# Performance work log

Hardware: AMD Instinct MI355X
Metric: run time of the kernel (lower is better)

## Reference

```python
import jax, jax.numpy as jnp
import numpy as np

B, L, H, N, VOCAB, OUT, NL = 16, 2048, 512, 64, 256, 256, 4
N2 = N // 2  # conjugate-symmetric half of the state


def setup_inputs() -> dict:
    key = jax.random.key(0)
    ks = jax.random.split(key, 8)
    x = jax.random.randint(ks[0], (B, L), 0, VOCAB)
    emb = jax.random.normal(ks[1], (VOCAB, H), jnp.float32)
    Ws = jax.random.normal(ks[2], (NL, H, H), jnp.float32) / np.float32(np.sqrt(H))
    bs = jnp.zeros((NL, H), jnp.float32)
    dt_min, dt_max = 1e-3, 1e-1
    log_dt = (jax.random.uniform(ks[3], (NL, H), jnp.float32)
              * np.float32(np.log(dt_max) - np.log(dt_min)) + np.float32(np.log(dt_min)))
    log_A_real = jnp.full((NL, H, N2), np.float32(np.log(0.5)), jnp.float32)
    A_imag = jnp.broadcast_to(np.float32(np.pi) * jnp.arange(N2, dtype=jnp.float32), (NL, H, N2))
    C_re = jax.random.normal(ks[4], (NL, H, N2), jnp.float32)
    C_im = jax.random.normal(ks[5], (NL, H, N2), jnp.float32)
    Ds = jax.random.normal(ks[6], (NL, H), jnp.float32)
    Wo = jax.random.normal(ks[7], (H, OUT), jnp.float32) / np.float32(np.sqrt(H))
    bo = jnp.zeros((OUT,), jnp.float32)
    return dict(x=x, emb=emb, Ws=Ws, bs=bs, log_dt=log_dt, log_A_real=log_A_real,
                A_imag=A_imag, C_re=C_re, C_im=C_im, Ds=Ds, Wo=Wo, bo=bo)


def _s4d(u, log_dt, log_A_real, A_imag, C_re, C_im, D):
    # u: (B, Lseq, H). Standard minimal S4D (diagonal SSM, ZOH-style kernel, FFT causal conv).
    Lseq = u.shape[1]
    dt = jnp.exp(log_dt)                      # (H,)
    A = -jnp.exp(log_A_real) + 1j * A_imag    # (H, N2) complex
    C = C_re + 1j * C_im                      # (H, N2)
    dtA = A * dt[:, None]                     # (H, N2)
    coef = C * (jnp.exp(dtA) - 1.0) / A       # (H, N2)
    # Vandermonde over time: exp(dtA * l), l = 0..L-1
    vand = jnp.exp(dtA[:, :, None] * jnp.arange(Lseq, dtype=jnp.float32))  # (H, N2, L)
    K = 2.0 * jnp.einsum('hn,hnl->hl', coef, vand).real                    # (H, L)
    ud = jnp.transpose(u, (0, 2, 1))          # (B, H, L)
    kf = jnp.fft.rfft(K, n=2 * Lseq)
    uf = jnp.fft.rfft(ud, n=2 * Lseq)
    y = jnp.fft.irfft(uf * kf, n=2 * Lseq)[..., :Lseq]  # causal conv
    y = y + D[:, None] * ud                   # skip connection
    return jnp.transpose(y, (0, 2, 1))        # (B, L, H)


def reference(x, emb, Ws, bs, log_dt, log_A_real, A_imag, C_re, C_im, Ds, Wo, bo):
    h = emb[x]  # (B, L, H)
    for i in range(NL):
        # every sub-layer gets the outer residual: x = layer(x) + x
        h = (h @ Ws[i] + bs[i]) + h           # Linear + residual
        h = jax.nn.relu(h) + h                # ReLU + residual
        h = h + h                             # Dropout (eval: identity) + residual
        h = _s4d(h, log_dt[i], log_A_real[i], A_imag[i], C_re[i], C_im[i], Ds[i]) + h
        h = jax.nn.relu(h) + h
        h = h + h
    return h @ Wo + bo
```

## Files before the change

### kernel.cpp

```cpp
#include <hip/hip_runtime.h>

#define BB 16
#define LL 2048
#define HH 512
#define NN2 32
#define NLAY 4
#define OUTD 256
#define BLM (BB*LL)
#define NELEM ((size_t)BLM*HH)
#define NC 16
#define LC (LL/NC)
#define LGLC 7

typedef __attribute__((ext_vector_type(8))) short s8v;
typedef __attribute__((ext_vector_type(4))) float f4v;

__device__ __forceinline__ unsigned short f2bf(float f) {
  unsigned u = __float_as_uint(f);
  return (unsigned short)((u + 0x7fffu + ((u >> 16) & 1u)) >> 16);
}
__device__ __forceinline__ float bf2f(unsigned short h) {
  return __uint_as_float((unsigned)h << 16);
}
__device__ __forceinline__ void gload16(const void* g, void* l) {
  __builtin_amdgcn_global_load_lds(
      (const __attribute__((address_space(1))) unsigned int*)g,
      (__attribute__((address_space(3))) unsigned int*)l, 16, 0, 0);
}

__global__ __launch_bounds__(256) void k_embed(const int* __restrict__ x,
    const float* __restrict__ emb, unsigned short* __restrict__ Ahi,
    unsigned short* __restrict__ Alo) {
  int idx = blockIdx.x * 256 + threadIdx.x;
  int j4 = idx & 127;
  int bl = idx >> 7;
  int tok = x[bl];
  float4 v = reinterpret_cast<const float4*>(emb)[tok * 128 + j4];
  unsigned short h0 = f2bf(v.x), h1 = f2bf(v.y), h2 = f2bf(v.z), h3 = f2bf(v.w);
  unsigned short l0 = f2bf(v.x - bf2f(h0)), l1 = f2bf(v.y - bf2f(h1));
  unsigned short l2 = f2bf(v.z - bf2f(h2)), l3 = f2bf(v.w - bf2f(h3));
  uint2 hp = make_uint2((unsigned)h0 | ((unsigned)h1 << 16),
                        (unsigned)h2 | ((unsigned)h3 << 16));
  uint2 lp = make_uint2((unsigned)l0 | ((unsigned)l1 << 16),
                        (unsigned)l2 | ((unsigned)l3 << 16));
  *reinterpret_cast<uint2*>(&Ahi[(size_t)idx * 4]) = hp;
  *reinterpret_cast<uint2*>(&Alo[(size_t)idx * 4]) = lp;
}

__global__ __launch_bounds__(256) void k_trans(const float* __restrict__ W, int N,
    unsigned short* __restrict__ th, unsigned short* __restrict__ tl) {
  int t = blockIdx.x * 256 + threadIdx.x;
  int k = t & 511, n = t >> 9;
  float v = W[(size_t)k * N + n];
  unsigned short hi = f2bf(v);
  th[(size_t)n * 512 + k] = hi;
  tl[(size_t)n * 512 + k] = f2bf(v - bf2f(hi));
}

__global__ __launch_bounds__(256) void k_params(const float* __restrict__ log_dt,
    const float* __restrict__ log_A_real, const float* __restrict__ A_imag,
    const float* __restrict__ C_re, const float* __restrict__ C_im,
    int layer, float4* __restrict__ par) {
  int idx = blockIdx.x * 256 + threadIdx.x;
  int h = idx >> 5;
  int o = layer * HH * NN2 + idx;
  float dt  = expf(log_dt[layer * HH + h]);
  float Are = -expf(log_A_real[o]);
  float Aim = A_imag[o];
  float er = expf(Are * dt);
  float lr = er * cosf(Aim * dt), li = er * sinf(Aim * dt);
  float inv  = 1.0f / (Are * Are + Aim * Aim);
  float numr = lr - 1.0f, numi = li;
  float qr = (numr * Are + numi * Aim) * inv;
  float qi = (numi * Are - numr * Aim) * inv;
  float cr = C_re[o], ci = C_im[o];
  par[idx] = make_float4(lr, li, 2.0f * (cr * qr - ci * qi),
                                 2.0f * (cr * qi + ci * qr));
}

template<int EPI>
__global__ __launch_bounds__(256) void k_gemm(
    const unsigned short* __restrict__ Ahi, const unsigned short* __restrict__ Alo,
    const unsigned short* __restrict__ Bhi, const unsigned short* __restrict__ Blo,
    const float* __restrict__ bias, float* __restrict__ Out, int N) {
  __shared__ short lds[32768];
  const int tid = threadIdx.x;
  const int lane = tid & 63, w = tid >> 6;
  const int wr = w >> 1, wc = w & 1;
  const int m0 = blockIdx.y * 128, n0 = blockIdx.x * 128;
  const int lm = lane & 15, lk = lane >> 4;

  const unsigned short* ga[2][2]; const unsigned short* gb[2][2];
  short *da[2][2], *db[2][2];
#pragma unroll
  for (int f2 = 0; f2 < 2; ++f2) {
    int f = w * 2 + f2;
    size_t ra = (size_t)(m0 + f * 16 + lm) * 512 + lk * 8;
    size_t rb = (size_t)(n0 + f * 16 + lm) * 512 + lk * 8;
    ga[0][f2] = Ahi + ra; ga[1][f2] = Alo + ra;
    gb[0][f2] = Bhi + rb; gb[1][f2] = Blo + rb;
    da[0][f2] = &lds[f * 512 + lane * 8];
    da[1][f2] = &lds[4096 + f * 512 + lane * 8];
    db[0][f2] = &lds[8192 + f * 512 + lane * 8];
    db[1][f2] = &lds[12288 + f * 512 + lane * 8];
  }
  f4v acc[4][4];
#pragma unroll
  for (int i = 0; i < 4; ++i)
#pragma unroll
    for (int j = 0; j < 4; ++j) acc[i][j] = (f4v){0.f, 0.f, 0.f, 0.f};

  auto stage = [&](int kt, int bofs) {
#pragma unroll
    for (int f2 = 0; f2 < 2; ++f2) {
      gload16(ga[0][f2] + kt * 32, da[0][f2] + bofs);
      gload16(ga[1][f2] + kt * 32, da[1][f2] + bofs);
      gload16(gb[0][f2] + kt * 32, db[0][f2] + bofs);
      gload16(gb[1][f2] + kt * 32, db[1][f2] + bofs);
    }
  };
  auto compute = [&](int bofs) {
    s8v ah[4], al[4], bh[4], bl[4];
#pragma unroll
    for (int i = 0; i < 4; ++i) {
      ah[i] = *(const s8v*)&lds[bofs + (wr * 4 + i) * 512 + lane * 8];
      al[i] = *(const s8v*)&lds[bofs + 4096 + (wr * 4 + i) * 512 + lane * 8];
      bh[i] = *(const s8v*)&lds[bofs + 8192 + (wc * 4 + i) * 512 + lane * 8];
      bl[i] = *(const s8v*)&lds[bofs + 12288 + (wc * 4 + i) * 512 + lane * 8];
    }
#pragma unroll
    for (int mi = 0; mi < 4; ++mi)
#pragma unroll
      for (int ni = 0; ni < 4; ++ni) {
        acc[mi][ni] = __builtin_amdgcn_mfma_f32_16x16x32_bf16(ah[mi], bh[ni], acc[mi][ni], 0, 0, 0);
        acc[mi][ni] = __builtin_amdgcn_mfma_f32_16x16x32_bf16(al[mi], bh[ni], acc[mi][ni], 0, 0, 0);
        acc[mi][ni] = __builtin_amdgcn_mfma_f32_16x16x32_bf16(ah[mi], bl[ni], acc[mi][ni], 0, 0, 0);
      }
  };

  stage(0, 0);
  __syncthreads();
#pragma unroll 1
  for (int t = 0; t < 8; ++t) {
    stage(2 * t + 1, 16384);
    compute(0);
    __syncthreads();
    if (t < 7) stage(2 * t + 2, 0);
    compute(16384);
    __syncthreads();
  }
  float bb[4];
#pragma unroll
  for (int ni = 0; ni < 4; ++ni) bb[ni] = bias[n0 + wc * 64 + ni * 16 + lm];
#pragma unroll
  for (int mi = 0; mi < 4; ++mi) {
#pragma unroll
    for (int r = 0; r < 4; ++r) {
      int row = m0 + wr * 64 + mi * 16 + lk * 4 + r;
      float* po = Out + (size_t)row * N;
      const unsigned short* ph = Ahi + (size_t)row * 512;
      const unsigned short* pl = Alo + (size_t)row * 512;
#pragma unroll
      for (int ni = 0; ni < 4; ++ni) {
        int col = n0 + wc * 64 + ni * 16 + lm;
        float t = acc[mi][ni][r] + bb[ni];
        if (EPI) {
          t += bf2f(ph[col]) + bf2f(pl[col]);
          t = t < 0.f ? 2.f * t : 4.f * t;
        }
        po[col] = t;
      }
    }
  }
}

__global__ __launch_bounds__(256) void k_sa(const float* __restrict__ U,
    const float4* __restrict__ par, float2* __restrict__ st) {
  int tid = threadIdx.x;
  int n = tid & 31, hs = tid >> 5;
  int hb = blockIdx.x, c = blockIdx.y, b = blockIdx.z;
  int h = (hb << 3) + hs;
  float4 p = par[(h << 5) + n];
  float lr = p.x, li = p.y;
  const float* Up = U + ((size_t)b * LL + (size_t)c * LC) * HH + h;
  float sr = 0.f, si = 0.f;
  auto step = [&](float uv) {
    float nsr = fmaf(lr, sr, fmaf(-li, si, uv));
    si = fmaf(lr, si, li * sr);
    sr = nsr;
  };
  float u0 = Up[0], u1 = Up[HH], u2 = Up[2 * HH], u3 = Up[3 * HH];
  for (int lg = 0; lg < LC / 4; ++lg) {
    const float* nx = Up + (size_t)(lg * 4 + 4) * HH;
    float v0 = nx[0], v1 = nx[HH], v2 = nx[2 * HH], v3 = nx[3 * HH];
    step(u0); step(u1); step(u2); step(u3);
    u0 = v0; u1 = v1; u2 = v2; u3 = v3;
  }
  st[(((size_t)b * (NC - 1) + c) * HH + h) * NN2 + n] = make_float2(sr, si);
}

__global__ __launch_bounds__(256) void k_fold(const float4* __restrict__ par,
    float2* __restrict__ st) {
  int t = blockIdx.x * 256 + threadIdx.x;
  int hn = t & 16383;
  int b = t >> 14;
  float4 p = par[hn];
  float ar = p.x, ai = p.y;
#pragma unroll
  for (int s = 0; s < LGLC; ++s) { float nr = ar * ar - ai * ai; ai = 2.f * ar * ai; ar = nr; }
  float gr = 0.f, gi = 0.f;
  size_t idx = (size_t)b * (NC - 1) * 16384 + hn;
  for (int c = 0; c < NC - 1; ++c) {
    float2 s = st[idx + (size_t)c * 16384];
    float ngr = fmaf(ar, gr, fmaf(-ai, gi, s.x));
    gi = fmaf(ar, gi, fmaf(ai, gr, s.y));
    gr = ngr;
    st[idx + (size_t)c * 16384] = make_float2(gr, gi);
  }
}

__global__ __launch_bounds__(256) void k_sb(const float* __restrict__ U,
    const float4* __restrict__ par, const float2* __restrict__ st,
    const float* __restrict__ D, unsigned short* __restrict__ Hhi,
    unsigned short* __restrict__ Hlo) {
  int tid = threadIdx.x;
  int q = tid & 3, hs = tid >> 2;
  int hb = blockIdx.x, c = blockIdx.y, b = blockIdx.z;
  int h = (hb << 6) + hs;
  float lr[8], li[8], cr[8], ci[8], tr[8], ti[8];
#pragma unroll
  for (int j = 0; j < 8; ++j) {
    float4 p = par[(h << 5) + (q << 3) + j];
    lr[j] = p.x; li[j] = p.y; cr[j] = p.z; ci[j] = p.w;
    tr[j] = 0.f; ti[j] = 0.f;
  }
  if (c > 0) {
#pragma unroll
    for (int j = 0; j < 8; ++j) {
      float2 s = st[(((size_t)b * (NC - 1) + (c - 1)) * HH + h) * NN2 + (q << 3) + j];
      tr[j] = cr[j] * s.x - ci[j] * s.y;
      ti[j] = cr[j] * s.y + ci[j] * s.x;
    }
  }
  float dp1 = D[h] + 1.0f;
  size_t base = ((size_t)b * LL + (size_t)c * LC) * HH + h;
  const float* Up = U + base;
  auto step = [&](float uv) -> float {
    float ys = 0.f;
#pragma unroll
    for (int j = 0; j < 8; ++j) {
      float ntr = fmaf(lr[j], tr[j], fmaf(-li[j], ti[j], cr[j] * uv));
      ti[j] = fmaf(lr[j], ti[j], fmaf(li[j], tr[j], ci[j] * uv));
      tr[j] = ntr;
      ys += ntr;
    }
    ys += __shfl_xor(ys, 1);
    ys += __shfl_xor(ys, 2);
    float t4 = fmaf(dp1, uv, ys);
    return t4 < 0.f ? 2.f * t4 : 4.f * t4;
  };
  float u0 = Up[0], u1 = Up[HH], u2 = Up[2 * HH], u3 = Up[3 * HH];
  for (int lg = 0; lg < LC / 4; ++lg) {
    const float* nx = Up + (size_t)(lg * 4 + 4) * HH;
    float v0 = nx[0], v1 = nx[HH], v2 = nx[2 * HH], v3 = nx[3 * HH];
    float r0 = step(u0), r1 = step(u1), r2 = step(u2), r3 = step(u3);
    float rq = q == 0 ? r0 : q == 1 ? r1 : q == 2 ? r2 : r3;
    size_t o = base + (size_t)(lg * 4 + q) * HH;
    unsigned short hi = f2bf(rq);
    Hhi[o] = hi;
    Hlo[o] = f2bf(rq - bf2f(hi));
    u0 = v0; u1 = v1; u2 = v2; u3 = v3;
  }
}

extern "C" void kernel_launch(void* const* d_in, const int* in_sizes, int n_in,
                              void* d_out, int out_size, void* d_ws, size_t ws_size,
                              hipStream_t stream) {
  const int*   x      = (const int*)d_in[0];
  const float* emb    = (const float*)d_in[1];
  const float* Ws     = (const float*)d_in[2];
  const float* bs     = (const float*)d_in[3];
  const float* log_dt = (const float*)d_in[4];
  const float* lAr    = (const float*)d_in[5];
  const float* Aim    = (const float*)d_in[6];
  const float* Cre    = (const float*)d_in[7];
  const float* Cim    = (const float*)d_in[8];
  const float* Ds     = (const float*)d_in[9];
  const float* Wo     = (const float*)d_in[10];
  const float* bo     = (const float*)d_in[11];

  float*          bufU   = (float*)d_ws;
  unsigned short* bufAhi = (unsigned short*)(bufU + NELEM);
  unsigned short* bufAlo = bufAhi + NELEM;
  float4*         par    = (float4*)(bufAlo + NELEM);
  float2*         st     = (float2*)(par + HH * NN2);
  unsigned short* wth    = (unsigned short*)(st + (size_t)BB * (NC - 1) * HH * NN2);
  unsigned short* wtl    = wth + 512 * 512;

  k_embed<<<(int)(NELEM / 4 / 256), 256, 0, stream>>>(x, emb, bufAhi, bufAlo);
  for (int i = 0; i < NLAY; ++i) {
    k_params<<<HH * NN2 / 256, 256, 0, stream>>>(log_dt, lAr, Aim, Cre, Cim, i, par);
    k_trans<<<HH * 512 / 256, 256, 0, stream>>>(Ws + (size_t)i * HH * HH, HH, wth, wtl);
    k_gemm<1><<<dim3(HH / 128, BLM / 128), 256, 0, stream>>>(
        bufAhi, bufAlo, wth, wtl, bs + i * HH, bufU, HH);
    k_sa<<<dim3(64, NC - 1, BB), 256, 0, stream>>>(bufU, par, st);
    k_fold<<<BB * HH * NN2 / 256, 256, 0, stream>>>(par, st);
    k_sb<<<dim3(8, NC, BB), 256, 0, stream>>>(bufU, par, st, Ds + i * HH, bufAhi, bufAlo);
  }
  k_trans<<<OUTD * 512 / 256, 256, 0, stream>>>(Wo, OUTD, wth, wtl);
  k_gemm<0><<<dim3(OUTD / 128, BLM / 128), 256, 0, stream>>>(
      bufAhi, bufAlo, wth, wtl, bo, (float*)d_out, OUTD);
}
```

Measured before the change: 1.189 ms.

## Assign all SSM modes of a channel to one thread in scan kernels

The chunked diagonal-SSM scan kernels now give each thread one channel and all 32 complex modes, instead of spreading modes across lanes. The parameter and state layouts become mode-major so per-channel accesses coalesce across threads. This removes redundant input loads and the cross-lane shuffle reduction, and lets each thread write four outputs. The cost is heavy register pressure and far fewer blocks and waves, which reduces latency hiding.

```diff
diff --git a/kernel.cpp b/kernel.cpp
--- a/kernel.cpp
+++ b/kernel.cpp
@@ -62,7 +62,7 @@
     const float* __restrict__ C_re, const float* __restrict__ C_im,
     int layer, float4* __restrict__ par) {
   int idx = blockIdx.x * 256 + threadIdx.x;
-  int h = idx >> 5;
+  int h = idx >> 5, n = idx & 31;
   int o = layer * HH * NN2 + idx;
   float dt  = expf(log_dt[layer * HH + h]);
   float Are = -expf(log_A_real[o]);
@@ -74,8 +74,8 @@
   float qr = (numr * Are + numi * Aim) * inv;
   float qi = (numi * Are - numr * Aim) * inv;
   float cr = C_re[o], ci = C_im[o];
-  par[idx] = make_float4(lr, li, 2.0f * (cr * qr - ci * qi),
-                                 2.0f * (cr * qi + ci * qr));
+  par[n * HH + h] = make_float4(lr, li, 2.0f * (cr * qr - ci * qi),
+                                        2.0f * (cr * qi + ci * qr));
 }
 
 template<int EPI>
@@ -174,20 +174,24 @@
   }
 }
 
-__global__ __launch_bounds__(256) void k_sa(const float* __restrict__ U,
+__global__ __launch_bounds__(256, 2) void k_sa(const float* __restrict__ U,
     const float4* __restrict__ par, float2* __restrict__ st) {
-  int tid = threadIdx.x;
-  int n = tid & 31, hs = tid >> 5;
-  int hb = blockIdx.x, c = blockIdx.y, b = blockIdx.z;
-  int h = (hb << 3) + hs;
-  float4 p = par[(h << 5) + n];
-  float lr = p.x, li = p.y;
+  int h = (blockIdx.x << 8) + threadIdx.x;
+  int c = blockIdx.y, b = blockIdx.z;
+  float lr[32], li[32], gr[32], gi[32];
+#pragma unroll
+  for (int n = 0; n < 32; ++n) {
+    float4 p = par[n * HH + h];
+    lr[n] = p.x; li[n] = p.y; gr[n] = 0.f; gi[n] = 0.f;
+  }
   const float* Up = U + ((size_t)b * LL + (size_t)c * LC) * HH + h;
-  float sr = 0.f, si = 0.f;
   auto step = [&](float uv) {
-    float nsr = fmaf(lr, sr, fmaf(-li, si, uv));
-    si = fmaf(lr, si, li * sr);
-    sr = nsr;
+#pragma unroll
+    for (int n = 0; n < 32; ++n) {
+      float ngr = fmaf(lr[n], gr[n], fmaf(-li[n], gi[n], uv));
+      gi[n] = fmaf(lr[n], gi[n], li[n] * gr[n]);
+      gr[n] = ngr;
+    }
   };
   float u0 = Up[0], u1 = Up[HH], u2 = Up[2 * HH], u3 = Up[3 * HH];
   for (int lg = 0; lg < LC / 4; ++lg) {
@@ -196,20 +200,23 @@
     step(u0); step(u1); step(u2); step(u3);
     u0 = v0; u1 = v1; u2 = v2; u3 = v3;
   }
-  st[(((size_t)b * (NC - 1) + c) * HH + h) * NN2 + n] = make_float2(sr, si);
+  size_t so = ((size_t)b * (NC - 1) + c) * (NN2 * HH) + h;
+#pragma unroll
+  for (int n = 0; n < 32; ++n)
+    st[so + (size_t)n * HH] = make_float2(gr[n], gi[n]);
 }
 
 __global__ __launch_bounds__(256) void k_fold(const float4* __restrict__ par,
     float2* __restrict__ st) {
   int t = blockIdx.x * 256 + threadIdx.x;
-  int hn = t & 16383;
+  int r = t & 16383;
   int b = t >> 14;
-  float4 p = par[hn];
+  float4 p = par[r];
   float ar = p.x, ai = p.y;
 #pragma unroll
   for (int s = 0; s < LGLC; ++s) { float nr = ar * ar - ai * ai; ai = 2.f * ar * ai; ar = nr; }
   float gr = 0.f, gi = 0.f;
-  size_t idx = (size_t)b * (NC - 1) * 16384 + hn;
+  size_t idx = (size_t)b * (NC - 1) * 16384 + r;
   for (int c = 0; c < NC - 1; ++c) {
     float2 s = st[idx + (size_t)c * 16384];
     float ngr = fmaf(ar, gr, fmaf(-ai, gi, s.x));
@@ -219,56 +226,58 @@
   }
 }
 
-__global__ __launch_bounds__(256) void k_sb(const float* __restrict__ U,
+__global__ __launch_bounds__(256, 2) void k_sb(const float* __restrict__ U,
     const float4* __restrict__ par, const float2* __restrict__ st,
     const float* __restrict__ D, unsigned short* __restrict__ Hhi,
     unsigned short* __restrict__ Hlo) {
-  int tid = threadIdx.x;
-  int q = tid & 3, hs = tid >> 2;
-  int hb = blockIdx.x, c = blockIdx.y, b = blockIdx.z;
-  int h = (hb << 6) + hs;
-  float lr[8], li[8], cr[8], ci[8], tr[8], ti[8];
-#pragma unroll
-  for (int j = 0; j < 8; ++j) {
-    float4 p = par[(h << 5) + (q << 3) + j];
-    lr[j] = p.x; li[j] = p.y; cr[j] = p.z; ci[j] = p.w;
-    tr[j] = 0.f; ti[j] = 0.f;
+  int h = (blockIdx.x << 8) + threadIdx.x;
+  int c = blockIdx.y, b = blockIdx.z;
+  float lr[32], li[32], cr[32], ci[32], tr[32], ti[32];
+#pragma unroll
+  for (int n = 0; n < 32; ++n) {
+    float4 p = par[n * HH + h];
+    lr[n] = p.x; li[n] = p.y; cr[n] = p.z; ci[n] = p.w;
+    tr[n] = 0.f; ti[n] = 0.f;
   }
   if (c > 0) {
-#pragma unroll
-    for (int j = 0; j < 8; ++j) {
-      float2 s = st[(((size_t)b * (NC - 1) + (c - 1)) * HH + h) * NN2 + (q << 3) + j];
-      tr[j] = cr[j] * s.x - ci[j] * s.y;
-      ti[j] = cr[j] * s.y + ci[j] * s.x;
+    size_t so = ((size_t)b * (NC - 1) + (c - 1)) * (NN2 * HH) + h;
+#pragma unroll
+    for (int n = 0; n < 32; ++n) {
+      float2 s = st[so + (size_t)n * HH];
+      tr[n] = cr[n] * s.x - ci[n] * s.y;
+      ti[n] = cr[n] * s.y + ci[n] * s.x;
     }
   }
   float dp1 = D[h] + 1.0f;
   size_t base = ((size_t)b * LL + (size_t)c * LC) * HH + h;
   const float* Up = U + base;
+  unsigned short* Hh = Hhi + base;
+  unsigned short* Hl = Hlo + base;
   auto step = [&](float uv) -> float {
-    float ys = 0.f;
-#pragma unroll
-    for (int j = 0; j < 8; ++j) {
-      float ntr = fmaf(lr[j], tr[j], fmaf(-li[j], ti[j], cr[j] * uv));
-      ti[j] = fmaf(lr[j], ti[j], fmaf(li[j], tr[j], ci[j] * uv));
-      tr[j] = ntr;
-      ys += ntr;
-    }
-    ys += __shfl_xor(ys, 1);
-    ys += __shfl_xor(ys, 2);
-    float t4 = fmaf(dp1, uv, ys);
+    float y0 = 0.f, y1 = 0.f, y2 = 0.f, y3 = 0.f;
+#pragma unroll
+    for (int n = 0; n < 32; ++n) {
+      float ntr = fmaf(lr[n], tr[n], fmaf(-li[n], ti[n], cr[n] * uv));
+      ti[n] = fmaf(lr[n], ti[n], fmaf(li[n], tr[n], ci[n] * uv));
+      tr[n] = ntr;
+      if ((n & 3) == 0) y0 += ntr; else if ((n & 3) == 1) y1 += ntr;
+      else if ((n & 3) == 2) y2 += ntr; else y3 += ntr;
+    }
+    float t4 = fmaf(dp1, uv, (y0 + y1) + (y2 + y3));
     return t4 < 0.f ? 2.f * t4 : 4.f * t4;
   };
   float u0 = Up[0], u1 = Up[HH], u2 = Up[2 * HH], u3 = Up[3 * HH];
   for (int lg = 0; lg < LC / 4; ++lg) {
     const float* nx = Up + (size_t)(lg * 4 + 4) * HH;
     float v0 = nx[0], v1 = nx[HH], v2 = nx[2 * HH], v3 = nx[3 * HH];
+    size_t o = (size_t)(lg * 4) * HH;
     float r0 = step(u0), r1 = step(u1), r2 = step(u2), r3 = step(u3);
-    float rq = q == 0 ? r0 : q == 1 ? r1 : q == 2 ? r2 : r3;
-    size_t o = base + (size_t)(lg * 4 + q) * HH;
-    unsigned short hi = f2bf(rq);
-    Hhi[o] = hi;
-    Hlo[o] = f2bf(rq - bf2f(hi));
+    unsigned short h0 = f2bf(r0), h1 = f2bf(r1), h2 = f2bf(r2), h3 = f2bf(r3);
+    Hh[o] = h0; Hh[o + HH] = h1; Hh[o + 2 * HH] = h2; Hh[o + 3 * HH] = h3;
+    Hl[o]          = f2bf(r0 - bf2f(h0));
+    Hl[o + HH]     = f2bf(r1 - bf2f(h1));
+    Hl[o + 2 * HH] = f2bf(r2 - bf2f(h2));
+    Hl[o + 3 * HH] = f2bf(r3 - bf2f(h3));
     u0 = v0; u1 = v1; u2 = v2; u3 = v3;
   }
 }
@@ -303,9 +312,9 @@
     k_trans<<<HH * 512 / 256, 256, 0, stream>>>(Ws + (size_t)i * HH * HH, HH, wth, wtl);
     k_gemm<1><<<dim3(HH / 128, BLM / 128), 256, 0, stream>>>(
         bufAhi, bufAlo, wth, wtl, bs + i * HH, bufU, HH);
-    k_sa<<<dim3(64, NC - 1, BB), 256, 0, stream>>>(bufU, par, st);
+    k_sa<<<dim3(2, NC - 1, BB), 256, 0, stream>>>(bufU, par, st);
     k_fold<<<BB * HH * NN2 / 256, 256, 0, stream>>>(par, st);
-    k_sb<<<dim3(8, NC, BB), 256, 0, stream>>>(bufU, par, st, Ds + i * HH, bufAhi, bufAlo);
+    k_sb<<<dim3(2, NC, BB), 256, 0, stream>>>(bufU, par, st, Ds + i * HH, bufAhi, bufAlo);
   }
   k_trans<<<OUTD * 512 / 256, 256, 0, stream>>>(Wo, OUTD, wth, wtl);
   k_gemm<0><<<dim3(OUTD / 128, BLM / 128), 256, 0, stream>>>(
```

Measured after the change: 3.139 ms. 164% more time.
